# Kernel optimization log

Hardware: AMD Instinct MI355X
Metric: run time of the kernel (lower is better)

The kernel has to match this reference:

```python
import jax, jax.numpy as jnp
import numpy as np

EPS = 1e-12  # tf/keras l2_normalize epsilon


def _hadamard(n):
    # Sylvester construction; n must be a power of 2
    H = np.array([[1.0]], dtype=np.float32)
    while H.shape[0] < n:
        H = np.block([[H, H], [H, -H]])
    return H


def setup_inputs() -> dict:
    key = jax.random.key(0)
    k1, k2 = jax.random.split(key)
    in_dim, out_dim, batch = 2048, 16384, 1024
    hadamard_size = 16384  # next pow2 of max(in_dim, out_dim)
    H = _hadamard(hadamard_size)[:in_dim, :out_dim]  # [2048, 16384]
    init_scale = 1.0 / np.sqrt(out_dim)
    x = jax.random.normal(k1, (batch, in_dim), dtype=jnp.float32)
    scale = jnp.full((1,), init_scale, dtype=jnp.float32)
    bias = jax.random.uniform(k2, (out_dim,), minval=-init_scale, maxval=init_scale, dtype=jnp.float32)
    return {"x": x, "scale": scale, "bias": bias, "hadamard": jnp.asarray(H)}


def reference(x, scale, bias, hadamard):
    # L2-normalize along features (keras: x / sqrt(max(sum(x^2), eps)))
    sq = jnp.sum(x * x, axis=-1, keepdims=True)
    xn = x * jax.lax.rsqrt(jnp.maximum(sq, EPS))
    # structured Hadamard matmul (expressed as dense GEMM, as in the original)
    out = -scale * jnp.matmul(xn, hadamard)  # [B, out_dim]
    out = out + bias
    return out
```

## Files before the change

### kernel.cpp

```cpp
#include <hip/hip_runtime.h>

#define IN_DIM   2048
#define OUT_DIM  16384
#define NT       256
#define EPS      1e-12f


__device__ __forceinline__ int swz(int e) { return e ^ (((e >> 6) & 7) << 3); }

#define BFLY(m)                                                   \
    _Pragma("unroll")                                             \
    for (int k = 0; k < 8; ++k)                                   \
        if (!(k & (m))) {                                         \
            const float a_ = v[k], b_ = v[k | (m)];               \
            v[k]       = a_ + b_;                                 \
            v[k | (m)] = a_ - b_;                                 \
        }

__global__ __launch_bounds__(NT, 4) void had_fwht_kernel(
    const float* __restrict__ x,
    const float* __restrict__ scale,
    const float* __restrict__ bias,
    float* __restrict__ out)
{
    __shared__ float sA[IN_DIM];
    __shared__ float sB[IN_DIM];
    __shared__ float red[NT / 64];

    const int b = blockIdx.x;
    const int t = threadIdx.x;
    const int l = t & 63;
    const int w = t >> 6;

    const float4* xr4 = (const float4*)(x + (size_t)b * IN_DIM);
    const float4 a0 = xr4[2 * t];
    const float4 a1 = xr4[2 * t + 1];

    const float4* bias4 = (const float4*)bias;
    float4 bj[16];
#pragma unroll
    for (int i = 0; i < 16; ++i) bj[i] = bias4[t + i * NT];

    const float negscale = -scale[0];

    float v[8] = {a0.x, a0.y, a0.z, a0.w, a1.x, a1.y, a1.z, a1.w};

    float local = 0.f;
#pragma unroll
    for (int k = 0; k < 8; ++k) local = fmaf(v[k], v[k], local);
#pragma unroll
    for (int off = 32; off > 0; off >>= 1)
        local += __shfl_down(local, off, 64);
    if (l == 0) red[w] = local;

    BFLY(1) BFLY(2) BFLY(4)

    {
        const int base = swz(t << 3);
        *(float4*)&sA[base]     = make_float4(v[0], v[1], v[2], v[3]);
        *(float4*)&sA[base + 4] = make_float4(v[4], v[5], v[6], v[7]);
    }
    const int bB = (w << 9) | ((l >> 3) << 6) | (l & 7);
#pragma unroll
    for (int k = 0; k < 8; ++k) v[k] = sA[swz(bB | (k << 3))];
    BFLY(1) BFLY(2) BFLY(4)

#pragma unroll
    for (int k = 0; k < 8; ++k) sA[swz(bB | (k << 3))] = v[k];
    const int bC = (w << 9) | l;
#pragma unroll
    for (int k = 0; k < 8; ++k) v[k] = sA[swz(bC | (k << 6))];
    BFLY(1) BFLY(2) BFLY(4)

#pragma unroll
    for (int k = 0; k < 8; ++k) sB[bC | (k << 6)] = v[k];

    asm volatile("s_waitcnt lgkmcnt(0)" ::: "memory");
    __builtin_amdgcn_s_barrier();

    const float sumsq = red[0] + red[1] + red[2] + red[3];
    const float c = negscale * rsqrtf(fmaxf(sumsq, EPS));

    const float4* sB4 = (const float4*)sB;
    const int q = t & 127;
    const float4 G0 = sB4[q];
    const float4 G1 = sB4[q + 128];
    const float4 G2 = sB4[q + 256];
    const float4 G3 = sB4[q + 384];

    float4 s01, d01, s23, d23;
    s01.x = G0.x + G1.x; s01.y = G0.y + G1.y; s01.z = G0.z + G1.z; s01.w = G0.w + G1.w;
    d01.x = G0.x - G1.x; d01.y = G0.y - G1.y; d01.z = G0.z - G1.z; d01.w = G0.w - G1.w;
    s23.x = G2.x + G3.x; s23.y = G2.y + G3.y; s23.z = G2.z + G3.z; s23.w = G2.w + G3.w;
    d23.x = G2.x - G3.x; d23.y = G2.y - G3.y; d23.z = G2.z - G3.z; d23.w = G2.w - G3.w;

    const bool hi = (t >= 128);
    const float4 A = hi ? d01 : s01;
    const float4 B = hi ? d23 : s23;
    float4 w_e, w_o;
    w_e.x = A.x + B.x; w_e.y = A.y + B.y; w_e.z = A.z + B.z; w_e.w = A.w + B.w;
    w_o.x = A.x - B.x; w_o.y = A.y - B.y; w_o.z = A.z - B.z; w_o.w = A.w - B.w;

    float4* orow = (float4*)(out + (size_t)b * OUT_DIM);
#pragma unroll
    for (int i = 0; i < 16; ++i) {
        const float4 ws = (i & 1) ? w_o : w_e;
        float4 o;
        o.x = fmaf(c, ws.x, bj[i].x);
        o.y = fmaf(c, ws.y, bj[i].y);
        o.z = fmaf(c, ws.z, bj[i].z);
        o.w = fmaf(c, ws.w, bj[i].w);
        orow[t + i * NT] = o;
    }
}

extern "C" void kernel_launch(void* const* d_in, const int* in_sizes, int n_in,
                              void* d_out, int out_size, void* d_ws, size_t ws_size,
                              hipStream_t stream) {
    const float* x     = (const float*)d_in[0];
    const float* scale = (const float*)d_in[1];
    const float* bias  = (const float*)d_in[2];
    float* out = (float*)d_out;

    const int batch = in_sizes[0] / IN_DIM;
    had_fwht_kernel<<<batch, NT, 0, stream>>>(x, scale, bias, out);
}
```

Before: 18.24 us.

## Split into row-WHT kernel and grid-stride bias-add expansion kernel

Splits the fused kernel in two. The first computes the 2048-wide WHT per row, scales it and writes a compact 2048-float result to workspace. The second is a grid-stride elementwise kernel that tiles this pattern across the 16384 outputs and adds the bias. The aim is to decouple the write-heavy expansion from the per-row transform for better parallelism and occupancy, at the cost of a second launch and an extra round trip of the 8 MB workspace through memory.

```diff
diff --git a/kernel.cpp b/kernel.cpp
--- a/kernel.cpp
+++ b/kernel.cpp
@@ -17,11 +17,10 @@
             v[k | (m)] = a_ - b_;                                 \
         }
 
-__global__ __launch_bounds__(NT, 4) void had_fwht_kernel(
+__global__ __launch_bounds__(NT, 4) void wht_rows_kernel(
     const float* __restrict__ x,
     const float* __restrict__ scale,
-    const float* __restrict__ bias,
-    float* __restrict__ out)
+    float* __restrict__ ws)
 {
     __shared__ float sA[IN_DIM];
     __shared__ float sB[IN_DIM];
@@ -35,11 +34,6 @@
     const float4* xr4 = (const float4*)(x + (size_t)b * IN_DIM);
     const float4 a0 = xr4[2 * t];
     const float4 a1 = xr4[2 * t + 1];
-
-    const float4* bias4 = (const float4*)bias;
-    float4 bj[16];
-#pragma unroll
-    for (int i = 0; i < 16; ++i) bj[i] = bias4[t + i * NT];
 
     const float negscale = -scale[0];
 
@@ -98,19 +92,38 @@
     const float4 A = hi ? d01 : s01;
     const float4 B = hi ? d23 : s23;
     float4 w_e, w_o;
-    w_e.x = A.x + B.x; w_e.y = A.y + B.y; w_e.z = A.z + B.z; w_e.w = A.w + B.w;
-    w_o.x = A.x - B.x; w_o.y = A.y - B.y; w_o.z = A.z - B.z; w_o.w = A.w - B.w;
+    w_e.x = c * (A.x + B.x); w_e.y = c * (A.y + B.y);
+    w_e.z = c * (A.z + B.z); w_e.w = c * (A.w + B.w);
+    w_o.x = c * (A.x - B.x); w_o.y = c * (A.y - B.y);
+    w_o.z = c * (A.z - B.z); w_o.w = c * (A.w - B.w);
 
-    float4* orow = (float4*)(out + (size_t)b * OUT_DIM);
-#pragma unroll
-    for (int i = 0; i < 16; ++i) {
-        const float4 ws = (i & 1) ? w_o : w_e;
+    float4* ws4 = (float4*)ws + ((size_t)b << 9);
+    ws4[t]       = w_e;
+    ws4[t + 256] = w_o;
+}
+
+__global__ __launch_bounds__(NT, 8) void expand_kernel(
+    const float* __restrict__ ws,
+    const float* __restrict__ bias,
+    float* __restrict__ out,
+    int total4)
+{
+    const float4* ws4   = (const float4*)ws;
+    const float4* bias4 = (const float4*)bias;
+    float4* out4        = (float4*)out;
+
+    const int stride = gridDim.x * NT;
+    for (int idx = blockIdx.x * NT + threadIdx.x; idx < total4; idx += stride) {
+        const int m4  = idx & 4095;
+        const int row = idx >> 12;
+        const float4 wv = ws4[(row << 9) | (m4 & 511)];
+        const float4 bv = bias4[m4];
         float4 o;
-        o.x = fmaf(c, ws.x, bj[i].x);
-        o.y = fmaf(c, ws.y, bj[i].y);
-        o.z = fmaf(c, ws.z, bj[i].z);
-        o.w = fmaf(c, ws.w, bj[i].w);
-        orow[t + i * NT] = o;
+        o.x = wv.x + bv.x;
+        o.y = wv.y + bv.y;
+        o.z = wv.z + bv.z;
+        o.w = wv.w + bv.w;
+        out4[idx] = o;
     }
 }
 
@@ -121,7 +134,11 @@
     const float* scale = (const float*)d_in[1];
     const float* bias  = (const float*)d_in[2];
     float* out = (float*)d_out;
+    float* ws  = (float*)d_ws;
 
     const int batch = in_sizes[0] / IN_DIM;
-    had_fwht_kernel<<<batch, NT, 0, stream>>>(x, scale, bias, out);
+    wht_rows_kernel<<<batch, NT, 0, stream>>>(x, scale, ws);
+
+    const int total4 = batch * (OUT_DIM / 4);
+    expand_kernel<<<2048, NT, 0, stream>>>(ws, bias, out, total4);
 }
```

New measurement: 30.29 us. +66.0%, slower.
